# Kernel tuning notes

Measured on AMD Instinct MI355X. Metric: run time of the kernel, lower is better.

The kernel has to match this reference:

```python
import jax, jax.numpy as jnp
import numpy as np

B, S, D, H = 2, 2048, 1024, 16
HD = D // H
EPS = 1e-5


def layer_norm(x, g, b):
    m = jnp.mean(x, axis=-1, keepdims=True)
    v = jnp.mean(jnp.square(x - m), axis=-1, keepdims=True)
    return (x - m) * jax.lax.rsqrt(v + EPS) * g + b


def setup_inputs() -> dict:
    key = jax.random.key(0)
    ks = jax.random.split(key, 16)
    s = 0.02
    x = jax.random.normal(ks[0], (B, S, D), dtype=jnp.float32)
    mask = jax.random.randint(ks[1], (1, 1, S, S), 0, 2, dtype=jnp.int32)
    return {
        "x": x,
        "mask": mask,
        "Wq": jax.random.normal(ks[2], (D, D), jnp.float32) * s,
        "Wk": jax.random.normal(ks[3], (D, D), jnp.float32) * s,
        "Wv": jax.random.normal(ks[4], (D, D), jnp.float32) * s,
        "Wo": jax.random.normal(ks[5], (D, D), jnp.float32) * s,
        "bo": jax.random.normal(ks[6], (D,), jnp.float32) * s,
        "ln1_g": jnp.ones((D,), jnp.float32),
        "ln1_b": jnp.zeros((D,), jnp.float32),
        "W1": jax.random.normal(ks[7], (D, 4 * D), jnp.float32) * s,
        "b1": jax.random.normal(ks[8], (4 * D,), jnp.float32) * s,
        "W2": jax.random.normal(ks[9], (4 * D, D), jnp.float32) * s,
        "b2": jax.random.normal(ks[10], (D,), jnp.float32) * s,
        "ln2_g": jnp.ones((D,), jnp.float32),
        "ln2_b": jnp.zeros((D,), jnp.float32),
    }


def reference(x, mask, Wq, Wk, Wv, Wo, bo, ln1_g, ln1_b, W1, b1, W2, b2, ln2_g, ln2_b):
    # --- multi-head attention (dropout = identity in eval) ---
    q = (x @ Wq).reshape(B, S, H, HD)
    k = (x @ Wk).reshape(B, S, H, HD)
    v = (x @ Wv).reshape(B, S, H, HD)
    scores = jnp.einsum("bshd,bthd->bhst", q, k) / jnp.sqrt(jnp.float32(HD))
    scores = jnp.where(mask == 1, jnp.float32(-1e9), scores)
    p = jax.nn.softmax(scores, axis=-1)
    o = jnp.einsum("bhst,bthd->bshd", p, v).reshape(B, S, D)
    attn_out = o @ Wo + bo
    # --- residual with norm on the branch (note: norm applied to attn output) ---
    x = x + layer_norm(attn_out, ln1_g, ln1_b)
    # --- FFN: gelu after fc1 AND after fc2 (as in source) ---
    h = jax.nn.gelu(x @ W1 + b1, approximate=False)
    h = jax.nn.gelu(h @ W2 + b2, approximate=False)
    x = x + layer_norm(h, ln2_g, ln2_b)
    return x
```

## Files before the change

kernel.cpp:

```cpp
#include <hip/hip_runtime.h>
#include <hip/hip_bf16.h>
#include <cstdint>

#define BB 2
#define SS 2048
#define DD 1024
#define HH 16
#define HDIM 64
#define MROWS (BB*SS)

typedef __bf16 bf16;
using bf16x8 = __bf16 __attribute__((ext_vector_type(8)));
using bf16x4 = __bf16 __attribute__((ext_vector_type(4)));
using bf16x2 = __bf16 __attribute__((ext_vector_type(2)));
using f32x4  = float __attribute__((ext_vector_type(4)));

__device__ __forceinline__ float gelu_exact(float x) {
    return 0.5f * x * (1.f + erff(x * 0.70710678118654752f));
}

__device__ __forceinline__ void stage16(const bf16* g, bf16* lds_chunk_base, int lane) {
#if __has_builtin(__builtin_amdgcn_global_load_lds)
    __builtin_amdgcn_global_load_lds((const __attribute__((address_space(1))) void*)g,
                                     (__attribute__((address_space(3))) void*)lds_chunk_base,
                                     16, 0, 0);
#else
    *(bf16x8*)(lds_chunk_base + lane * 8) = *(const bf16x8*)g;
#endif
}

__global__ __launch_bounds__(256) void prep_kernel(
    const float* __restrict__ x, bf16* __restrict__ x_b,
    const int* __restrict__ mask, unsigned long long* __restrict__ maskb,
    const float* __restrict__ Wq, const float* __restrict__ Wk,
    const float* __restrict__ Wv, const float* __restrict__ Wo,
    const float* __restrict__ W1, const float* __restrict__ W2,
    bf16* __restrict__ Wqkv_t, bf16* __restrict__ Wo_t,
    bf16* __restrict__ W1_t, bf16* __restrict__ W2_t) {
    const int bid = blockIdx.x;
    if (bid < 4096) {
        int i = bid * 256 + threadIdx.x;
        float4 v = ((const float4*)x)[i];
        bf16x4 o;
        o[0] = (bf16)v.x; o[1] = (bf16)v.y; o[2] = (bf16)v.z; o[3] = (bf16)v.w;
        *(bf16x4*)(x_b + (size_t)i * 4) = o;
        return;
    }
    if (bid < 20480) {
        int gid = (bid - 4096) * 256 + threadIdx.x;
        int mv = mask[gid];
        unsigned long long bal = __ballot(mv == 1);
        if ((threadIdx.x & 63) == 0) maskb[gid >> 6] = bal;
        return;
    }
    int t = bid - 20480;
    const float* W; bf16* Wt; int K, N, bx, by;
    if (t < 4096) {
        int wsel = t >> 10;
        int tt = t & 1023;
        W  = (wsel == 0) ? Wq : (wsel == 1) ? Wk : (wsel == 2) ? Wv : Wo;
        Wt = (wsel == 3) ? Wo_t : (Wqkv_t + (size_t)wsel * 1024 * 1024);
        K = 1024; N = 1024; bx = (tt & 31) * 32; by = (tt >> 5) * 32;
    } else if (t < 8192) {
        int tt = t - 4096;
        W = W1; Wt = W1_t; K = 1024; N = 4096;
        bx = (tt & 127) * 32; by = (tt >> 7) * 32;
    } else {
        int tt = t - 8192;
        W = W2; Wt = W2_t; K = 4096; N = 1024;
        bx = (tt & 31) * 32; by = (tt >> 5) * 32;
    }
    __shared__ float tile[32][33];
    int tx = threadIdx.x & 31;
    int ty = threadIdx.x >> 5;
#pragma unroll
    for (int j = 0; j < 4; ++j)
        tile[ty + j * 8][tx] = W[(size_t)(by + ty + j * 8) * N + bx + tx];
    __syncthreads();
#pragma unroll
    for (int j = 0; j < 4; ++j)
        Wt[(size_t)(bx + ty + j * 8) * K + by + tx] = (bf16)tile[tx][ty + j * 8];
}

template <int EPI>
__global__ __launch_bounds__(256, 3) void gemm_bt(const bf16* __restrict__ A,
                                                  const bf16* __restrict__ Bt,
                                                  void* __restrict__ C,
                                                  const float* __restrict__ bias,
                                                  int M, int N, int K) {
    __shared__ __align__(16) bf16 As[128 * 64];
    __shared__ __align__(16) bf16 Bs[128 * 64];
    const int tid  = threadIdx.x;
    const int lane = tid & 63;
    const int wave = tid >> 6;
    const int l16  = lane & 15;
    const int quad = lane >> 4;
    const int wm = wave >> 1, wn = wave & 1;
    const int m0 = blockIdx.y * 128, n0 = blockIdx.x * 128;

    f32x4 acc[4][4];
#pragma unroll
    for (int i = 0; i < 4; ++i)
#pragma unroll
        for (int j = 0; j < 4; ++j) acc[i][j] = (f32x4){0.f, 0.f, 0.f, 0.f};

    const int nsteps = K >> 6;
    for (int kt = 0; kt < nsteps; ++kt) {
        const int kbase = kt << 6;
#pragma unroll
        for (int c = 0; c < 4; ++c) {
            int chunk = wave * 4 + c;
            int gi = chunk * 64 + lane;
            int m  = gi >> 3;
            int cp = gi & 7;
            int g  = cp ^ (m & 7);
            stage16(A  + (size_t)(m0 + m) * K + kbase + g * 8, As + chunk * 512, lane);
            stage16(Bt + (size_t)(n0 + m) * K + kbase + g * 8, Bs + chunk * 512, lane);
        }
        __syncthreads();
#pragma unroll
        for (int ks = 0; ks < 2; ++ks) {
            bf16x8 af[4], bfr[4];
#pragma unroll
            for (int i = 0; i < 4; ++i) {
                int m = wm * 64 + i * 16 + l16;
                int g = ks * 4 + quad;
                af[i]  = *(const bf16x8*)(As + m * 64 + ((g ^ (m & 7)) * 8));
                int n = wn * 64 + i * 16 + l16;
                bfr[i] = *(const bf16x8*)(Bs + n * 64 + ((g ^ (n & 7)) * 8));
            }
#pragma unroll
            for (int i = 0; i < 4; ++i)
#pragma unroll
                for (int j = 0; j < 4; ++j)
                    acc[i][j] = __builtin_amdgcn_mfma_f32_16x16x32_bf16(af[i], bfr[j], acc[i][j], 0, 0, 0);
        }
        __syncthreads();
    }

#pragma unroll
    for (int i = 0; i < 4; ++i) {
        int row = m0 + wm * 64 + i * 16 + quad * 4;
#pragma unroll
        for (int j = 0; j < 4; ++j) {
            int col = n0 + wn * 64 + j * 16 + l16;
            float bv = (EPI != 0) ? bias[col] : 0.f;
#pragma unroll
            for (int r = 0; r < 4; ++r) {
                float v = acc[i][j][r];
                if (EPI != 0) v += bv;
                if (EPI >= 2) v = gelu_exact(v);
                size_t idx = (size_t)(row + r) * N + col;
                if (EPI == 0 || EPI == 2) ((bf16*)C)[idx] = (bf16)v;
                else                      ((float*)C)[idx] = v;
            }
        }
    }
}

__global__ __launch_bounds__(256) void flash_attn(const bf16* __restrict__ qkv,
                                                  const unsigned long long* __restrict__ maskb,
                                                  bf16* __restrict__ o) {
    __shared__ __align__(16) bf16 Ks[128 * 64];
    __shared__ __align__(16) bf16 Vts[64 * 136];
    const int tid  = threadIdx.x;
    const int lane = tid & 63;
    const int wave = tid >> 6;
    const int l16  = lane & 15;
    const int quad = lane >> 4;
    const int bh = blockIdx.y;
    const int b = bh >> 4, h = bh & 15;
    const int q0 = blockIdx.x * 64;
    const size_t rowb = (size_t)b * SS;
    const float SCL = 0.18033688011112042f;

    const size_t qrow = (rowb + q0 + wave * 16 + l16) * 3072 + h * 64;
    bf16x8 qf[2];
    qf[0] = *(const bf16x8*)(qkv + qrow + quad * 8);
    qf[1] = *(const bf16x8*)(qkv + qrow + 32 + quad * 8);

    f32x4 oacc[4];
#pragma unroll
    for (int d = 0; d < 4; ++d) oacc[d] = (f32x4){0.f, 0.f, 0.f, 0.f};
    float lsum = 0.f;
    const int mrow32 = (q0 + wave * 16 + l16) * 32;

    const int vt_tc = (lane >> 4) * 32 + ((lane >> 1) & 3) * 8 + ((lane >> 3) & 1) * 4 + 2 * (lane & 1);

    for (int kt = 0; kt < SS / 128; ++kt) {
        const int t0 = kt * 128;
        ulonglong2 mw = *(const ulonglong2*)(maskb + mrow32 + kt * 2);
        __syncthreads();
#pragma unroll
        for (int c = 0; c < 4; ++c) {
            int chunk = wave * 4 + c;
            int gi = chunk * 64 + lane;
            int t  = gi >> 3;
            int cp = gi & 7;
            int g  = cp ^ (t & 7);
            stage16(qkv + (rowb + t0 + t) * 3072 + 1024 + h * 64 + g * 8, Ks + chunk * 512, lane);
        }
#pragma unroll
        for (int c = 0; c < 2; ++c) {
            int d8 = (wave + 4 * c) * 8;
            const bf16* vg = qkv + (rowb + t0 + 2 * lane) * 3072 + 2048 + h * 64 + d8;
            bf16x8 v0 = *(const bf16x8*)(vg);
            bf16x8 v1 = *(const bf16x8*)(vg + 3072);
#pragma unroll
            for (int j = 0; j < 8; ++j) {
                bf16x2 pr; pr[0] = v0[j]; pr[1] = v1[j];
                *(bf16x2*)(Vts + (d8 + j) * 136 + vt_tc) = pr;
            }
        }
        __syncthreads();

        f32x4 st[8];
#pragma unroll
        for (int tg = 0; tg < 8; ++tg) {
            int tl = tg * 16 + l16;
            bf16x8 a0 = *(const bf16x8*)(Ks + tl * 64 + ((quad       ^ (tl & 7)) * 8));
            bf16x8 a1 = *(const bf16x8*)(Ks + tl * 64 + (((4 + quad) ^ (tl & 7)) * 8));
            f32x4 s = (f32x4){0.f, 0.f, 0.f, 0.f};
            s = __builtin_amdgcn_mfma_f32_16x16x32_bf16(a0, qf[0], s, 0, 0, 0);
            s = __builtin_amdgcn_mfma_f32_16x16x32_bf16(a1, qf[1], s, 0, 0, 0);
            st[tg] = s;
        }
        unsigned long long s0 = mw.x >> (quad * 4);
        unsigned long long s1 = mw.y >> (quad * 4);
        bf16x8 pva[4];
#pragma unroll
        for (int tg = 0; tg < 8; ++tg) {
            unsigned int bits = (unsigned int)(((tg < 4) ? s0 : s1) >> ((tg & 3) * 16));
#pragma unroll
            for (int r = 0; r < 4; ++r) {
                float p = __builtin_amdgcn_exp2f(st[tg][r] * SCL);
                p = ((bits >> r) & 1u) ? 0.f : p;
                lsum += p;
                pva[tg >> 1][(tg & 1) * 4 + r] = (bf16)p;
            }
        }
#pragma unroll
        for (int kc = 0; kc < 4; ++kc) {
#pragma unroll
            for (int dg = 0; dg < 4; ++dg) {
                bf16x8 bfrag = *(const bf16x8*)(Vts + (dg * 16 + l16) * 136 + kc * 32 + quad * 8);
                oacc[dg] = __builtin_amdgcn_mfma_f32_16x16x32_bf16(pva[kc], bfrag, oacc[dg], 0, 0, 0);
            }
        }
    }

    lsum += __shfl_xor(lsum, 16, 64);
    lsum += __shfl_xor(lsum, 32, 64);
#pragma unroll
    for (int r = 0; r < 4; ++r) {
        float lr = __shfl(lsum, quad * 4 + r, 64);
        float inv_l = 1.f / lr;
        bf16* orow = o + (rowb + q0 + wave * 16 + quad * 4 + r) * DD + h * 64;
#pragma unroll
        for (int dg = 0; dg < 4; ++dg)
            orow[dg * 16 + l16] = (bf16)(oacc[dg][r] * inv_l);
    }
}

template <bool WB16>
__global__ __launch_bounds__(256) void ln_residual(const float* __restrict__ resid,
                                                   const float* __restrict__ a,
                                                   const float* __restrict__ g,
                                                   const float* __restrict__ bb,
                                                   float* __restrict__ outf,
                                                   bf16* __restrict__ outb) {
    const int row = blockIdx.x;
    const int tid = threadIdx.x;
    const size_t base = (size_t)row * DD + tid * 4;
    float4 av = *(const float4*)(a + base);
    float s1 = av.x + av.y + av.z + av.w;
    float s2 = av.x * av.x + av.y * av.y + av.z * av.z + av.w * av.w;
#pragma unroll
    for (int off = 32; off; off >>= 1) {
        s1 += __shfl_xor(s1, off, 64);
        s2 += __shfl_xor(s2, off, 64);
    }
    __shared__ float red[8];
    if ((tid & 63) == 0) { red[(tid >> 6) * 2] = s1; red[(tid >> 6) * 2 + 1] = s2; }
    __syncthreads();
    s1 = red[0] + red[2] + red[4] + red[6];
    s2 = red[1] + red[3] + red[5] + red[7];
    float mean = s1 * (1.f / DD);
    float var  = s2 * (1.f / DD) - mean * mean;
    float rs = rsqrtf(var + 1e-5f);
    float4 gv = *(const float4*)(g + tid * 4);
    float4 bv = *(const float4*)(bb + tid * 4);
    float4 rv = *(const float4*)(resid + base);
    float y0 = rv.x + (av.x - mean) * rs * gv.x + bv.x;
    float y1 = rv.y + (av.y - mean) * rs * gv.y + bv.y;
    float y2 = rv.z + (av.z - mean) * rs * gv.z + bv.z;
    float y3 = rv.w + (av.w - mean) * rs * gv.w + bv.w;
    float4 yo = make_float4(y0, y1, y2, y3);
    *(float4*)(outf + base) = yo;
    if (WB16) {
        bf16x4 ob;
        ob[0] = (bf16)y0; ob[1] = (bf16)y1; ob[2] = (bf16)y2; ob[3] = (bf16)y3;
        *(bf16x4*)(outb + base) = ob;
    }
}

extern "C" void kernel_launch(void* const* d_in, const int* in_sizes, int n_in,
                              void* d_out, int out_size, void* d_ws, size_t ws_size,
                              hipStream_t stream) {
    const float* x    = (const float*)d_in[0];
    const int*   mask = (const int*)d_in[1];
    const float* Wq   = (const float*)d_in[2];
    const float* Wk   = (const float*)d_in[3];
    const float* Wv   = (const float*)d_in[4];
    const float* Wo   = (const float*)d_in[5];
    const float* bo   = (const float*)d_in[6];
    const float* ln1g = (const float*)d_in[7];
    const float* ln1b = (const float*)d_in[8];
    const float* W1   = (const float*)d_in[9];
    const float* b1   = (const float*)d_in[10];
    const float* W2   = (const float*)d_in[11];
    const float* b2   = (const float*)d_in[12];
    const float* ln2g = (const float*)d_in[13];
    const float* ln2b = (const float*)d_in[14];

    char* w = (char*)d_ws;
    bf16* Wqkv_t = (bf16*)w; w += (size_t)3072 * 1024 * 2;
    bf16* Wo_t   = (bf16*)w; w += (size_t)1024 * 1024 * 2;
    bf16* W1_t   = (bf16*)w; w += (size_t)4096 * 1024 * 2;
    bf16* W2_t   = (bf16*)w; w += (size_t)1024 * 4096 * 2;
    bf16* x_b    = (bf16*)w; w += (size_t)MROWS * DD * 2;
    bf16* qkv    = (bf16*)w; w += (size_t)MROWS * 3072 * 2;
    float* attn_f = (float*)w; w += (size_t)MROWS * DD * 4;
    float* x1_f   = (float*)w; w += (size_t)MROWS * DD * 4;
    unsigned long long* maskb = (unsigned long long*)w; w += (size_t)SS * 32 * 8;
    bf16* o_b  = x_b;
    bf16* x1_b = x_b;
    bf16* h_b  = qkv;
    float* h2_f = (float*)d_out;

    prep_kernel<<<32768, 256, 0, stream>>>(x, x_b, mask, maskb,
                                           Wq, Wk, Wv, Wo, W1, W2,
                                           Wqkv_t, Wo_t, W1_t, W2_t);

    gemm_bt<0><<<dim3(3072 / 128, MROWS / 128), 256, 0, stream>>>(x_b, Wqkv_t, qkv, nullptr, MROWS, 3072, 1024);
    flash_attn<<<dim3(SS / 64, BB * HH), 256, 0, stream>>>(qkv, maskb, o_b);
    gemm_bt<1><<<dim3(1024 / 128, MROWS / 128), 256, 0, stream>>>(o_b, Wo_t, attn_f, bo, MROWS, 1024, 1024);
    ln_residual<true><<<MROWS, 256, 0, stream>>>(x, attn_f, ln1g, ln1b, x1_f, x1_b);
    gemm_bt<2><<<dim3(4096 / 128, MROWS / 128), 256, 0, stream>>>(x1_b, W1_t, h_b, b1, MROWS, 4096, 1024);
    gemm_bt<3><<<dim3(1024 / 128, MROWS / 128), 256, 0, stream>>>(h_b, W2_t, h2_f, b2, MROWS, 1024, 4096);
    ln_residual<false><<<MROWS, 256, 0, stream>>>(x1_f, h2_f, ln2g, ln2b, (float*)d_out, nullptr);
}
```

Before: 425.0 us.

## Split-K the N=1024 GEMMs and fuse bias/GELU into LayerNorm; prefetch V in attention

The Wo and W2 GEMMs, which launch only 256 blocks, are split into two K-halves along blockIdx.z. Each half writes fp32 partials to a separate buffer. The LayerNorm kernel then sums the partials, adds the bias, applies GELU where needed, and normalizes, so the block count doubles and CU utilization should improve. Flash attention now register-prefetches the next tile's V and mask words so global latency overlaps the compute. The cost is extra fp32 partial traffic and more registers in the attention kernel.

```diff
diff --git a/kernel.cpp b/kernel.cpp
--- a/kernel.cpp
+++ b/kernel.cpp
@@ -86,8 +86,9 @@
 __global__ __launch_bounds__(256, 3) void gemm_bt(const bf16* __restrict__ A,
                                                   const bf16* __restrict__ Bt,
                                                   void* __restrict__ C,
+                                                  void* __restrict__ C2,
                                                   const float* __restrict__ bias,
-                                                  int M, int N, int K) {
+                                                  int M, int N, int K, int ldk) {
     __shared__ __align__(16) bf16 As[128 * 64];
     __shared__ __align__(16) bf16 Bs[128 * 64];
     const int tid  = threadIdx.x;
@@ -97,6 +98,9 @@
     const int quad = lane >> 4;
     const int wm = wave >> 1, wn = wave & 1;
     const int m0 = blockIdx.y * 128, n0 = blockIdx.x * 128;
+    const int z  = blockIdx.z;
+    A  += (size_t)z * K;
+    Bt += (size_t)z * K;
 
     f32x4 acc[4][4];
 #pragma unroll
@@ -114,8 +118,8 @@
             int m  = gi >> 3;
             int cp = gi & 7;
             int g  = cp ^ (m & 7);
-            stage16(A  + (size_t)(m0 + m) * K + kbase + g * 8, As + chunk * 512, lane);
-            stage16(Bt + (size_t)(n0 + m) * K + kbase + g * 8, Bs + chunk * 512, lane);
+            stage16(A  + (size_t)(m0 + m) * ldk + kbase + g * 8, As + chunk * 512, lane);
+            stage16(Bt + (size_t)(n0 + m) * ldk + kbase + g * 8, Bs + chunk * 512, lane);
         }
         __syncthreads();
 #pragma unroll
@@ -138,21 +142,21 @@
         __syncthreads();
     }
 
+    float* Cz = (EPI == 4) ? (z ? (float*)C2 : (float*)C) : nullptr;
 #pragma unroll
     for (int i = 0; i < 4; ++i) {
         int row = m0 + wm * 64 + i * 16 + quad * 4;
 #pragma unroll
         for (int j = 0; j < 4; ++j) {
             int col = n0 + wn * 64 + j * 16 + l16;
-            float bv = (EPI != 0) ? bias[col] : 0.f;
+            float bv = (EPI == 2) ? bias[col] : 0.f;
 #pragma unroll
             for (int r = 0; r < 4; ++r) {
                 float v = acc[i][j][r];
-                if (EPI != 0) v += bv;
-                if (EPI >= 2) v = gelu_exact(v);
+                if (EPI == 2) v = gelu_exact(v + bv);
                 size_t idx = (size_t)(row + r) * N + col;
-                if (EPI == 0 || EPI == 2) ((bf16*)C)[idx] = (bf16)v;
-                else                      ((float*)C)[idx] = v;
+                if (EPI == 4) Cz[idx] = v;
+                else          ((bf16*)C)[idx] = (bf16)v;
             }
         }
     }
@@ -186,10 +190,19 @@
     const int mrow32 = (q0 + wave * 16 + l16) * 32;
 
     const int vt_tc = (lane >> 4) * 32 + ((lane >> 1) & 3) * 8 + ((lane >> 3) & 1) * 4 + 2 * (lane & 1);
+    const bf16* vbase = qkv + (rowb + 2 * lane) * 3072 + 2048 + h * 64;
+
+    bf16x8 pv0[2], pv1[2];
+#pragma unroll
+    for (int c = 0; c < 2; ++c) {
+        int d8 = (wave + 4 * c) * 8;
+        pv0[c] = *(const bf16x8*)(vbase + d8);
+        pv1[c] = *(const bf16x8*)(vbase + 3072 + d8);
+    }
+    ulonglong2 mw = *(const ulonglong2*)(maskb + mrow32);
 
     for (int kt = 0; kt < SS / 128; ++kt) {
         const int t0 = kt * 128;
-        ulonglong2 mw = *(const ulonglong2*)(maskb + mrow32 + kt * 2);
         __syncthreads();
 #pragma unroll
         for (int c = 0; c < 4; ++c) {
@@ -203,16 +216,26 @@
 #pragma unroll
         for (int c = 0; c < 2; ++c) {
             int d8 = (wave + 4 * c) * 8;
-            const bf16* vg = qkv + (rowb + t0 + 2 * lane) * 3072 + 2048 + h * 64 + d8;
-            bf16x8 v0 = *(const bf16x8*)(vg);
-            bf16x8 v1 = *(const bf16x8*)(vg + 3072);
 #pragma unroll
             for (int j = 0; j < 8; ++j) {
-                bf16x2 pr; pr[0] = v0[j]; pr[1] = v1[j];
+                bf16x2 pr; pr[0] = pv0[c][j]; pr[1] = pv1[c][j];
                 *(bf16x2*)(Vts + (d8 + j) * 136 + vt_tc) = pr;
             }
         }
         __syncthreads();
+
+        bf16x8 nv0[2], nv1[2];
+        ulonglong2 mwn;
+        if (kt + 1 < SS / 128) {
+            const bf16* vgn = vbase + (size_t)(t0 + 128) * 3072;
+#pragma unroll
+            for (int c = 0; c < 2; ++c) {
+                int d8 = (wave + 4 * c) * 8;
+                nv0[c] = *(const bf16x8*)(vgn + d8);
+                nv1[c] = *(const bf16x8*)(vgn + 3072 + d8);
+            }
+            mwn = *(const ulonglong2*)(maskb + mrow32 + (kt + 1) * 2);
+        }
 
         f32x4 st[8];
 #pragma unroll
@@ -247,6 +270,11 @@
                 oacc[dg] = __builtin_amdgcn_mfma_f32_16x16x32_bf16(pva[kc], bfrag, oacc[dg], 0, 0, 0);
             }
         }
+        if (kt + 1 < SS / 128) {
+#pragma unroll
+            for (int c = 0; c < 2; ++c) { pv0[c] = nv0[c]; pv1[c] = nv1[c]; }
+            mw = mwn;
+        }
     }
 
     lsum += __shfl_xor(lsum, 16, 64);
@@ -262,19 +290,28 @@
     }
 }
 
-template <bool WB16>
-__global__ __launch_bounds__(256) void ln_residual(const float* __restrict__ resid,
-                                                   const float* __restrict__ a,
-                                                   const float* __restrict__ g,
-                                                   const float* __restrict__ bb,
-                                                   float* __restrict__ outf,
-                                                   bf16* __restrict__ outb) {
+template <bool GELU, bool WB16>
+__global__ __launch_bounds__(256) void ln_fused(const float* __restrict__ resid,
+                                                const float* __restrict__ p0,
+                                                const float* __restrict__ p1,
+                                                const float* __restrict__ bias,
+                                                const float* __restrict__ g,
+                                                const float* __restrict__ bb,
+                                                float* __restrict__ outf,
+                                                bf16* __restrict__ outb) {
     const int row = blockIdx.x;
     const int tid = threadIdx.x;
     const size_t base = (size_t)row * DD + tid * 4;
-    float4 av = *(const float4*)(a + base);
-    float s1 = av.x + av.y + av.z + av.w;
-    float s2 = av.x * av.x + av.y * av.y + av.z * av.z + av.w * av.w;
+    float4 a0 = *(const float4*)(p0 + base);
+    float4 a1 = *(const float4*)(p1 + base);
+    float4 bz = *(const float4*)(bias + tid * 4);
+    float ax = a0.x + a1.x + bz.x;
+    float ay = a0.y + a1.y + bz.y;
+    float az = a0.z + a1.z + bz.z;
+    float aw = a0.w + a1.w + bz.w;
+    if (GELU) { ax = gelu_exact(ax); ay = gelu_exact(ay); az = gelu_exact(az); aw = gelu_exact(aw); }
+    float s1 = ax + ay + az + aw;
+    float s2 = ax * ax + ay * ay + az * az + aw * aw;
 #pragma unroll
     for (int off = 32; off; off >>= 1) {
         s1 += __shfl_xor(s1, off, 64);
@@ -291,10 +328,10 @@
     float4 gv = *(const float4*)(g + tid * 4);
     float4 bv = *(const float4*)(bb + tid * 4);
     float4 rv = *(const float4*)(resid + base);
-    float y0 = rv.x + (av.x - mean) * rs * gv.x + bv.x;
-    float y1 = rv.y + (av.y - mean) * rs * gv.y + bv.y;
-    float y2 = rv.z + (av.z - mean) * rs * gv.z + bv.z;
-    float y3 = rv.w + (av.w - mean) * rs * gv.w + bv.w;
+    float y0 = rv.x + (ax - mean) * rs * gv.x + bv.x;
+    float y1 = rv.y + (ay - mean) * rs * gv.y + bv.y;
+    float y2 = rv.z + (az - mean) * rs * gv.z + bv.z;
+    float y3 = rv.w + (aw - mean) * rs * gv.w + bv.w;
     float4 yo = make_float4(y0, y1, y2, y3);
     *(float4*)(outf + base) = yo;
     if (WB16) {
@@ -330,23 +367,26 @@
     bf16* W2_t   = (bf16*)w; w += (size_t)1024 * 4096 * 2;
     bf16* x_b    = (bf16*)w; w += (size_t)MROWS * DD * 2;
     bf16* qkv    = (bf16*)w; w += (size_t)MROWS * 3072 * 2;
-    float* attn_f = (float*)w; w += (size_t)MROWS * DD * 4;
-    float* x1_f   = (float*)w; w += (size_t)MROWS * DD * 4;
+    float* R     = (float*)w; w += (size_t)MROWS * DD * 8;
+    float* x1_f  = (float*)w; w += (size_t)MROWS * DD * 4;
     unsigned long long* maskb = (unsigned long long*)w; w += (size_t)SS * 32 * 8;
     bf16* o_b  = x_b;
     bf16* x1_b = x_b;
-    bf16* h_b  = qkv;
-    float* h2_f = (float*)d_out;
+    float* op0 = R;
+    float* op1 = R + (size_t)MROWS * DD;
+    bf16*  h_b = (bf16*)R;
+    float* fp0 = (float*)d_out;
+    float* fp1 = (float*)qkv;
 
     prep_kernel<<<32768, 256, 0, stream>>>(x, x_b, mask, maskb,
                                            Wq, Wk, Wv, Wo, W1, W2,
                                            Wqkv_t, Wo_t, W1_t, W2_t);
 
-    gemm_bt<0><<<dim3(3072 / 128, MROWS / 128), 256, 0, stream>>>(x_b, Wqkv_t, qkv, nullptr, MROWS, 3072, 1024);
+    gemm_bt<0><<<dim3(24, 32, 1), 256, 0, stream>>>(x_b, Wqkv_t, qkv, nullptr, nullptr, MROWS, 3072, 1024, 1024);
     flash_attn<<<dim3(SS / 64, BB * HH), 256, 0, stream>>>(qkv, maskb, o_b);
-    gemm_bt<1><<<dim3(1024 / 128, MROWS / 128), 256, 0, stream>>>(o_b, Wo_t, attn_f, bo, MROWS, 1024, 1024);
-    ln_residual<true><<<MROWS, 256, 0, stream>>>(x, attn_f, ln1g, ln1b, x1_f, x1_b);
-    gemm_bt<2><<<dim3(4096 / 128, MROWS / 128), 256, 0, stream>>>(x1_b, W1_t, h_b, b1, MROWS, 4096, 1024);
-    gemm_bt<3><<<dim3(1024 / 128, MROWS / 128), 256, 0, stream>>>(h_b, W2_t, h2_f, b2, MROWS, 1024, 4096);
-    ln_residual<false><<<MROWS, 256, 0, stream>>>(x1_f, h2_f, ln2g, ln2b, (float*)d_out, nullptr);
-}
+    gemm_bt<4><<<dim3(8, 32, 2), 256, 0, stream>>>(o_b, Wo_t, op0, op1, nullptr, MROWS, 1024, 512, 1024);
+    ln_fused<false, true><<<MROWS, 256, 0, stream>>>(x, op0, op1, bo, ln1g, ln1b, x1_f, x1_b);
+    gemm_bt<2><<<dim3(32, 32, 1), 256, 0, stream>>>(x1_b, W1_t, h_b, nullptr, b1, MROWS, 4096, 1024, 1024);
+    gemm_bt<4><<<dim3(8, 32, 2), 256, 0, stream>>>(h_b, W2_t, fp0, fp1, nullptr, MROWS, 1024, 2048, 4096);
+    ln_fused<true, false><<<MROWS, 256, 0, stream>>>(x1_f, fp0, fp1, b2, ln2g, ln2b, (float*)d_out, nullptr);
+}
```

Result: faster. 408.0 us (-4.0%).
